# Kernel tuning notes

Hardware: AMD Instinct MI355X
Metric: run time of the kernel (lower is better)

The kernel has to match this reference:

```python
import jax, jax.numpy as jnp
import numpy as np
import math

DIMS = [2048, 1024, 512, 4096]
NH, DK, DV = 16, 64, 64
BS = 8192
D_MODEL = NH * DK  # 1024


def setup_inputs() -> dict:
    key = jax.random.key(0)
    ks = jax.random.split(key, 3 * len(DIMS) + 5)
    inp = {"input_data": jax.random.normal(ks[0], (BS, sum(DIMS)), jnp.float32)}
    ki = 1
    for i, d in enumerate(DIMS):
        inp[f"wq{i}"] = jax.random.normal(ks[ki], (NH * DK, d), jnp.float32) * 0.02; ki += 1
        inp[f"wk{i}"] = jax.random.normal(ks[ki], (NH * DK, d), jnp.float32) * 0.02; ki += 1
        inp[f"wv{i}"] = jax.random.normal(ks[ki], (NH * DV, d), jnp.float32) * 0.02; ki += 1
    inp["fc_w"] = jax.random.normal(ks[ki], (NH * DV, NH * DV), jnp.float32) * 0.02; ki += 1
    inp["fc_b"] = jax.random.normal(ks[ki], (NH * DV,), jnp.float32) * 0.02; ki += 1
    inp["ln_g"] = jnp.ones((NH * DV,), jnp.float32)
    inp["ln_b"] = jnp.zeros((NH * DV,), jnp.float32)
    return inp


def _forward(input_data, wqs, wks, wvs, fc_w, fc_b, ln_g, ln_b):
    bs = input_data.shape[0]
    M = len(DIMS)
    offs = np.cumsum([0] + DIMS)
    # per-modality projections; stack into [bs, M, NH*D]
    xs = [input_data[:, offs[i]:offs[i + 1]] for i in range(M)]
    q = jnp.stack([x @ w.T for x, w in zip(xs, wqs)], axis=1)  # [bs, M, NH*DK]
    k = jnp.stack([x @ w.T for x, w in zip(xs, wks)], axis=1)
    v = jnp.stack([x @ w.T for x, w in zip(xs, wvs)], axis=1)  # [bs, M, NH*DV]
    residual = v  # v.transpose(1,2).view == original stacked v
    qh = q.reshape(bs, M, NH, DK).transpose(0, 2, 1, 3)  # [bs, NH, M, DK]
    kh = k.reshape(bs, M, NH, DK).transpose(0, 2, 1, 3)
    vh = v.reshape(bs, M, NH, DV).transpose(0, 2, 1, 3)
    scores = jnp.einsum('bhqd,bhkd->bhqk', qh, kh) / math.sqrt(DK)
    attn = jax.nn.softmax(scores, axis=-1)  # [bs, NH, M, M]
    ctx = jnp.einsum('bhqk,bhkd->bhqd', attn, vh)  # [bs, NH, M, DV]
    ctx = ctx.transpose(0, 2, 1, 3).reshape(bs, M, NH * DV)
    out = ctx @ fc_w.T + fc_b  # dropout is identity (p=0 / eval)
    out = out + residual
    mu = jnp.mean(out, axis=-1, keepdims=True)
    var = jnp.var(out, axis=-1, keepdims=True)
    out = (out - mu) / jnp.sqrt(var + 1e-6) * ln_g + ln_b
    return out, attn


def reference(input_data, wq0, wk0, wv0, wq1, wk1, wv1, wq2, wk2, wv2,
              wq3, wk3, wv3, fc_w, fc_b, ln_g, ln_b):
    wqs = [wq0, wq1, wq2, wq3]
    wks = [wk0, wk1, wk2, wk3]
    wvs = [wv0, wv1, wv2, wv3]
    return _forward(input_data, wqs, wks, wvs, fc_w, fc_b, ln_g, ln_b)
```

## Files before the change

kernel.cpp:

```cpp
#include <hip/hip_runtime.h>


typedef unsigned short u16;
typedef short short8 __attribute__((ext_vector_type(8)));
typedef float f32x4 __attribute__((ext_vector_type(4)));

__device__ __forceinline__ u16 f2bf(float f) {
  unsigned u = __builtin_bit_cast(unsigned, f);
  u += 0x7FFFu + ((u >> 16) & 1u);
  return (u16)(u >> 16);
}
__device__ __forceinline__ float bf2f(u16 s) {
  return __builtin_bit_cast(float, ((unsigned)s) << 16);
}

__device__ __forceinline__ void gload16(const u16* g, u16* l) {
  __builtin_amdgcn_global_load_lds(
      (const __attribute__((address_space(1))) void*)g,
      (__attribute__((address_space(3))) void*)l, 16, 0, 0);
}

#define CFENCE asm volatile("" ::: "memory")

struct CArgs {
  const float* src[14];
  unsigned long dst[14];
  int blk0[14];
  int n4[14];
};

__global__ __launch_bounds__(256) void convall(CArgs a, u16* __restrict__ wsb) {
  int blk = blockIdx.x;
  int s = 0;
#pragma unroll
  for (int i = 1; i < 14; ++i) s = (blk >= a.blk0[i]) ? i : s;
  int li = (blk - a.blk0[s]) * 256 + threadIdx.x;
  if (li < a.n4[s]) {
    float4 v = ((const float4*)a.src[s])[li];
    ushort4 o;
    o.x = f2bf(v.x); o.y = f2bf(v.y); o.z = f2bf(v.z); o.w = f2bf(v.w);
    ((ushort4*)(wsb + a.dst[s]))[li] = o;
  }
}

template <int MODE>
__global__ __launch_bounds__(512, 2)
void gemm8(const u16* __restrict__ Abase, int lda,
           const u16* __restrict__ Wbase, u16* __restrict__ Cq,
           u16* __restrict__ Cpre, const float* __restrict__ bias,
           const u16* __restrict__ resid) {
  __shared__ __align__(16) u16 lds[65536];

  const int tid = threadIdx.x;
  const int w = tid >> 6, lane = tid & 63;
  const int lr = lane & 15, lk = lane >> 4;
  const int wm = w >> 2, wn = w & 3;

  int K, nt, bx, by, coff;
  const u16 *A, *B;
  if (MODE == 0) {
    int seg = blockIdx.x / 384;
    int r = blockIdx.x % 384;
    bx = r % 12; by = r / 12;
    K = 4096 >> seg; nt = 64 >> seg;
    int xo, wo, mod;
    switch (seg) {
      case 0:  xo = 3584; wo = 11010048; mod = 3; break;
      case 1:  xo = 0;    wo = 0;        mod = 0; break;
      case 2:  xo = 2048; wo = 6291456;  mod = 1; break;
      default: xo = 3072; wo = 9437184;  mod = 2; break;
    }
    coff = mod * 3072;
    A = Abase + xo;
    B = Wbase + wo;
  } else {
    bx = blockIdx.x & 3; by = blockIdx.x >> 2;
    K = 1024; nt = 16; coff = 0;
    A = Abase; B = Wbase;
  }
  const size_t brow = (size_t)by * 256;
  const int bcol = bx * 256;
  const u16* Ab = A + brow * (size_t)lda;
  const u16* Bb = B + (size_t)bcol * (size_t)K;

  f32x4 acc[8][4];
#pragma unroll
  for (int i = 0; i < 8; ++i)
#pragma unroll
    for (int j = 0; j < 4; ++j) acc[i][j] = (f32x4){0.f, 0.f, 0.f, 0.f};

  auto stageA = [&](int p, int half) {
    const int base = (p & 1) * 65536 + half * 16384;
    const int k0 = p * 64;
#pragma unroll
    for (int l = 0; l < 2; ++l) {
      int s = l * 8192 + tid * 16;
      int rw = s >> 7;
      int ck = ((s >> 4) & 7) ^ (rw & 7);
      int row = (rw & 63) + ((rw >> 6) << 7) + half * 64;
      gload16(Ab + (size_t)row * lda + k0 + ck * 8, &lds[(base + s) >> 1]);
    }
  };
  auto stageB = [&](int p, int half) {
    const int base = (p & 1) * 65536 + 32768 + half * 16384;
    const int k0 = p * 64;
#pragma unroll
    for (int l = 0; l < 2; ++l) {
      int s = l * 8192 + tid * 16;
      int rw = s >> 7;
      int ck = ((s >> 4) & 7) ^ (rw & 7);
      int col = (rw & 31) + ((rw >> 5) << 6) + half * 32;
      gload16(Bb + (size_t)col * (size_t)K + k0 + ck * 8, &lds[(base + s) >> 1]);
    }
  };

  auto ldA = [&](int t, int half, short8* dst) {
    const u16* lp = lds + (((t & 1) * 65536 + half * 16384) >> 1);
#pragma unroll
    for (int mi = 0; mi < 4; ++mi) {
      int rw = mi * 16 + lr + wm * 64;
#pragma unroll
      for (int ks = 0; ks < 2; ++ks) {
        int pc = (ks * 4 + lk) ^ (rw & 7);
        dst[mi * 2 + ks] = *(const short8*)(lp + rw * 64 + pc * 8);
      }
    }
  };
  auto ldB = [&](int t, int half, short8* dst) {
    const u16* lp = lds + (((t & 1) * 65536 + 32768 + half * 16384) >> 1);
#pragma unroll
    for (int ni = 0; ni < 2; ++ni) {
      int rw = ni * 16 + lr + wn * 32;
#pragma unroll
      for (int ks = 0; ks < 2; ++ks) {
        int pc = (ks * 4 + lk) ^ (rw & 7);
        dst[ni * 2 + ks] = *(const short8*)(lp + rw * 64 + pc * 8);
      }
    }
  };

  short8 af[8], bl[4], bh[4];
  auto MQ = [&](short8* a, short8* b, int mo, int no) {
#pragma unroll
    for (int mi = 0; mi < 4; ++mi)
#pragma unroll
      for (int ni = 0; ni < 2; ++ni) {
        acc[mo + mi][no + ni] = __builtin_amdgcn_mfma_f32_16x16x32_bf16(
            a[mi * 2 + 0], b[ni * 2 + 0], acc[mo + mi][no + ni], 0, 0, 0);
        acc[mo + mi][no + ni] = __builtin_amdgcn_mfma_f32_16x16x32_bf16(
            a[mi * 2 + 1], b[ni * 2 + 1], acc[mo + mi][no + ni], 0, 0, 0);
      }
  };

  stageA(0, 0); stageB(0, 0); stageB(0, 1); stageA(0, 1);
  asm volatile("s_waitcnt vmcnt(4)" ::: "memory");
  __builtin_amdgcn_s_barrier();
  CFENCE;

#pragma unroll 1
  for (int t = 0; t < nt; ++t) {
    const bool more = (t + 1 < nt);
    ldA(t, 0, af);
    ldB(t, 0, bl);
    if (more) stageA(t + 1, 0);
    CFENCE;
    __builtin_amdgcn_s_barrier();
    asm volatile("s_waitcnt lgkmcnt(0)" ::: "memory");
    __builtin_amdgcn_sched_barrier(0);
    __builtin_amdgcn_s_setprio(1);
    MQ(af, bl, 0, 0);
    __builtin_amdgcn_s_setprio(0);
    CFENCE;
    if (more) asm volatile("s_waitcnt vmcnt(4)" ::: "memory");
    else      asm volatile("s_waitcnt vmcnt(2)" ::: "memory");
    __builtin_amdgcn_s_barrier();
    CFENCE;
    ldB(t, 1, bh);
    if (more) stageB(t + 1, 0);
    CFENCE;
    __builtin_amdgcn_s_barrier();
    asm volatile("s_waitcnt lgkmcnt(0)" ::: "memory");
    __builtin_amdgcn_sched_barrier(0);
    __builtin_amdgcn_s_setprio(1);
    MQ(af, bh, 0, 2);
    __builtin_amdgcn_s_setprio(0);
    CFENCE;
    if (more) asm volatile("s_waitcnt vmcnt(4)" ::: "memory");
    else      asm volatile("s_waitcnt vmcnt(0)" ::: "memory");
    __builtin_amdgcn_s_barrier();
    CFENCE;
    ldA(t, 1, af);
    if (more) stageB(t + 1, 1);
    CFENCE;
    __builtin_amdgcn_s_barrier();
    asm volatile("s_waitcnt lgkmcnt(0)" ::: "memory");
    __builtin_amdgcn_sched_barrier(0);
    __builtin_amdgcn_s_setprio(1);
    MQ(af, bh, 4, 2);
    __builtin_amdgcn_s_setprio(0);
    CFENCE;
    __builtin_amdgcn_s_barrier();
    CFENCE;
    if (more) stageA(t + 1, 1);
    CFENCE;
    __builtin_amdgcn_s_barrier();
    __builtin_amdgcn_s_setprio(1);
    MQ(af, bl, 4, 0);
    __builtin_amdgcn_s_setprio(0);
    CFENCE;
    if (more) {
      asm volatile("s_waitcnt vmcnt(4)" ::: "memory");
      __builtin_amdgcn_s_barrier();
      CFENCE;
    }
  }

  if (MODE == 0) {
#pragma unroll
    for (int mi = 0; mi < 8; ++mi)
#pragma unroll
      for (int ni = 0; ni < 4; ++ni) {
        const int c = coff + bcol + wn * 64 + ni * 16 + lr;
#pragma unroll
        for (int j = 0; j < 4; ++j) {
          size_t r = brow + wm * 128 + mi * 16 + lk * 4 + j;
          Cq[r * 12288 + c] = f2bf(acc[mi][ni][j]);
        }
      }
  } else {
#pragma unroll
    for (int mi = 0; mi < 8; ++mi)
#pragma unroll
      for (int ni = 0; ni < 4; ++ni) {
        const int c = bcol + wn * 64 + ni * 16 + lr;
        const float bs = bias[c];
#pragma unroll
        for (int j = 0; j < 4; ++j) {
          size_t r = brow + wm * 128 + mi * 16 + lk * 4 + j;
          size_t ridx = (r >> 2) * 12288 + (r & 3) * 3072 + 2048 + c;
          Cpre[r * 1024 + c] = f2bf(acc[mi][ni][j] + bs + bf2f(resid[ridx]));
        }
      }
  }
}

__global__ __launch_bounds__(256) void attn_k(const u16* __restrict__ qkv,
                                              u16* __restrict__ ctxb,
                                              float* __restrict__ attn_out) {
  const int tid = threadIdx.x;
  const int l = tid & 63;
  const int wg = blockIdx.x * 4 + (tid >> 6);
  const int b = wg >> 2;
  const int h0 = (wg & 3) << 2;
  const size_t base = (size_t)b * 12288 + h0 * 64 + l * 4;

  float q[4][4], k[4][4], v[4][4];
#pragma unroll
  for (int m = 0; m < 4; ++m) {
    ushort4 uq = *(const ushort4*)(qkv + base + m * 3072);
    ushort4 uk = *(const ushort4*)(qkv + base + m * 3072 + 1024);
    ushort4 uv = *(const ushort4*)(qkv + base + m * 3072 + 2048);
    q[m][0] = bf2f(uq.x); q[m][1] = bf2f(uq.y); q[m][2] = bf2f(uq.z); q[m][3] = bf2f(uq.w);
    k[m][0] = bf2f(uk.x); k[m][1] = bf2f(uk.y); k[m][2] = bf2f(uk.z); k[m][3] = bf2f(uk.w);
    v[m][0] = bf2f(uv.x); v[m][1] = bf2f(uv.y); v[m][2] = bf2f(uv.z); v[m][3] = bf2f(uv.w);
  }

  float s[16];
#pragma unroll
  for (int i = 0; i < 4; ++i)
#pragma unroll
    for (int j = 0; j < 4; ++j) {
      float acc = q[i][0] * k[j][0];
      acc += q[i][1] * k[j][1];
      acc += q[i][2] * k[j][2];
      acc += q[i][3] * k[j][3];
      s[i * 4 + j] = acc;
    }
#pragma unroll
  for (int off = 1; off < 16; off <<= 1) {
#pragma unroll
    for (int t = 0; t < 16; ++t) s[t] += __shfl_xor(s[t], off);
  }

  float a[16];
#pragma unroll
  for (int i = 0; i < 4; ++i) {
    float s0 = s[i * 4 + 0] * 0.125f, s1 = s[i * 4 + 1] * 0.125f;
    float s2 = s[i * 4 + 2] * 0.125f, s3 = s[i * 4 + 3] * 0.125f;
    float m = fmaxf(fmaxf(s0, s1), fmaxf(s2, s3));
    float e0 = __expf(s0 - m), e1 = __expf(s1 - m);
    float e2 = __expf(s2 - m), e3 = __expf(s3 - m);
    float inv = 1.0f / (e0 + e1 + e2 + e3);
    a[i * 4 + 0] = e0 * inv; a[i * 4 + 1] = e1 * inv;
    a[i * 4 + 2] = e2 * inv; a[i * 4 + 3] = e3 * inv;
  }

#pragma unroll
  for (int i = 0; i < 4; ++i) {
    float c0 = a[i*4+0]*v[0][0] + a[i*4+1]*v[1][0] + a[i*4+2]*v[2][0] + a[i*4+3]*v[3][0];
    float c1 = a[i*4+0]*v[0][1] + a[i*4+1]*v[1][1] + a[i*4+2]*v[2][1] + a[i*4+3]*v[3][1];
    float c2 = a[i*4+0]*v[0][2] + a[i*4+1]*v[1][2] + a[i*4+2]*v[2][2] + a[i*4+3]*v[3][2];
    float c3 = a[i*4+0]*v[0][3] + a[i*4+1]*v[1][3] + a[i*4+2]*v[2][3] + a[i*4+3]*v[3][3];
    ushort4 o;
    o.x = f2bf(c0); o.y = f2bf(c1); o.z = f2bf(c2); o.w = f2bf(c3);
    *(ushort4*)(ctxb + (size_t)b * 4096 + i * 1024 + h0 * 64 + l * 4) = o;
  }

  int sel = l & 15;
  float val = a[0];
#pragma unroll
  for (int t = 1; t < 16; ++t) val = (sel == t) ? a[t] : val;
  attn_out[(size_t)b * 256 + h0 * 16 + l] = val;
}

__global__ __launch_bounds__(256) void ln_k(const u16* __restrict__ pre,
                                            const float* __restrict__ g,
                                            const float* __restrict__ b,
                                            float* __restrict__ out) {
  int row = blockIdx.x;
  int tid = threadIdx.x;
  ushort4 u = *(const ushort4*)(pre + (size_t)row * 1024 + tid * 4);
  float x0 = bf2f(u.x), x1 = bf2f(u.y), x2 = bf2f(u.z), x3 = bf2f(u.w);
  float s = x0 + x1 + x2 + x3;
  float s2 = x0 * x0 + x1 * x1 + x2 * x2 + x3 * x3;
#pragma unroll
  for (int off = 32; off; off >>= 1) {
    s += __shfl_xor(s, off);
    s2 += __shfl_xor(s2, off);
  }
  __shared__ float r1[4], r2[4];
  int w = tid >> 6, lane = tid & 63;
  if (lane == 0) { r1[w] = s; r2[w] = s2; }
  __syncthreads();
  s = r1[0] + r1[1] + r1[2] + r1[3];
  s2 = r2[0] + r2[1] + r2[2] + r2[3];
  float mu = s * (1.0f / 1024.0f);
  float inv = rsqrtf(s2 * (1.0f / 1024.0f) - mu * mu + 1e-6f);
  float4 gv = *(const float4*)(g + tid * 4);
  float4 bv = *(const float4*)(b + tid * 4);
  float4 o;
  o.x = (x0 - mu) * inv * gv.x + bv.x;
  o.y = (x1 - mu) * inv * gv.y + bv.y;
  o.z = (x2 - mu) * inv * gv.z + bv.z;
  o.w = (x3 - mu) * inv * gv.w + bv.w;
  *(float4*)(out + (size_t)row * 1024 + tid * 4) = o;
}

extern "C" void kernel_launch(void* const* d_in, const int* in_sizes, int n_in,
                              void* d_out, int out_size, void* d_ws,
                              size_t ws_size, hipStream_t stream) {
  const float* fcb = (const float*)d_in[14];
  const float* lng = (const float*)d_in[15];
  const float* lnb = (const float*)d_in[16];

  u16* wsb = (u16*)d_ws;
  u16* xb = wsb;
  u16* wb = xb + 62914560;
  u16* qkv = wb + 24641536;
  u16* ctxb = qkv + 100663296;
  u16* pre = wsb;
  float* outp = (float*)d_out;
  float* attn_out = outp + 33554432;

  static const unsigned long woff[13] = {
      0,        2097152,  4194304,
      6291456,  7340032,  8388608,
      9437184,  9961472,  10485760,
      11010048, 15204352, 19398656,
      23592960};
  static const int wn4[13] = {524288, 524288, 524288, 262144, 262144, 262144,
                              131072, 131072, 131072, 1048576, 1048576, 1048576,
                              262144};

  CArgs ca;
  ca.src[0] = (const float*)d_in[0];
  ca.dst[0] = 0;
  ca.n4[0] = 62914560 / 4;
  ca.blk0[0] = 0;
  int nb = ca.n4[0] / 256;
  for (int i = 0; i < 13; ++i) {
    ca.src[i + 1] = (const float*)d_in[1 + i];
    ca.dst[i + 1] = 62914560ul + woff[i];
    ca.n4[i + 1] = wn4[i];
    ca.blk0[i + 1] = nb;
    nb += (wn4[i] + 255) / 256;
  }
  convall<<<dim3(nb), 256, 0, stream>>>(ca, wsb);

  gemm8<0><<<dim3(1536), 512, 0, stream>>>(xb, 7680, wb, qkv, nullptr, nullptr,
                                           nullptr);

  attn_k<<<dim3(8192), 256, 0, stream>>>(qkv, ctxb, attn_out);

  gemm8<1><<<dim3(512), 512, 0, stream>>>(ctxb, 1024, wb + 23592960, nullptr,
                                          pre, fcb, qkv);

  ln_k<<<dim3(32768), 256, 0, stream>>>(pre, lng, lnb, outp);
}
```

Baseline: 617.0 us.

## Switch GEMM to 32x32x16 MFMA and use nontemporal loads/stores throughout

The GEMM inner product moves from 16x16x32 to 32x32x16 bf16 MFMA instructions. LDS fragment loads and the epilogue indexing are reworked to match the 32x32 output layout, with fewer and larger accumulator tiles. Separately, streaming global loads and stores in the conversion, attention, LayerNorm and GEMM epilogue kernels become nontemporal to cut cache pollution. The larger MFMA reduces instruction count and LDS reads per flop. The epilogue still issues scalar 16-bit stores with a strided row pattern, and the nontemporal hints could hurt if data such as qkv would otherwise be reused from cache.

```diff
diff --git a/kernel.cpp b/kernel.cpp
--- a/kernel.cpp
+++ b/kernel.cpp
@@ -3,7 +3,9 @@
 
 typedef unsigned short u16;
 typedef short short8 __attribute__((ext_vector_type(8)));
+typedef unsigned short u16x4 __attribute__((ext_vector_type(4)));
 typedef float f32x4 __attribute__((ext_vector_type(4)));
+typedef float f32x16 __attribute__((ext_vector_type(16)));
 
 __device__ __forceinline__ u16 f2bf(float f) {
   unsigned u = __builtin_bit_cast(unsigned, f);
@@ -36,10 +38,10 @@
   for (int i = 1; i < 14; ++i) s = (blk >= a.blk0[i]) ? i : s;
   int li = (blk - a.blk0[s]) * 256 + threadIdx.x;
   if (li < a.n4[s]) {
-    float4 v = ((const float4*)a.src[s])[li];
-    ushort4 o;
+    f32x4 v = __builtin_nontemporal_load((const f32x4*)a.src[s] + li);
+    u16x4 o;
     o.x = f2bf(v.x); o.y = f2bf(v.y); o.z = f2bf(v.z); o.w = f2bf(v.w);
-    ((ushort4*)(wsb + a.dst[s]))[li] = o;
+    __builtin_nontemporal_store(o, (u16x4*)(wsb + a.dst[s]) + li);
   }
 }
 
@@ -53,7 +55,7 @@
 
   const int tid = threadIdx.x;
   const int w = tid >> 6, lane = tid & 63;
-  const int lr = lane & 15, lk = lane >> 4;
+  const int l31 = lane & 31, lk5 = lane >> 5;
   const int wm = w >> 2, wn = w & 3;
 
   int K, nt, bx, by, coff;
@@ -83,11 +85,11 @@
   const u16* Ab = A + brow * (size_t)lda;
   const u16* Bb = B + (size_t)bcol * (size_t)K;
 
-  f32x4 acc[8][4];
-#pragma unroll
-  for (int i = 0; i < 8; ++i)
-#pragma unroll
-    for (int j = 0; j < 4; ++j) acc[i][j] = (f32x4){0.f, 0.f, 0.f, 0.f};
+  f32x16 acc[4][2];
+#pragma unroll
+  for (int i = 0; i < 4; ++i)
+#pragma unroll
+    for (int j = 0; j < 2; ++j) acc[i][j] = (f32x16)(0.f);
 
   auto stageA = [&](int p, int half) {
     const int base = (p & 1) * 65536 + half * 16384;
@@ -117,39 +119,33 @@
   auto ldA = [&](int t, int half, short8* dst) {
     const u16* lp = lds + (((t & 1) * 65536 + half * 16384) >> 1);
 #pragma unroll
-    for (int mi = 0; mi < 4; ++mi) {
-      int rw = mi * 16 + lr + wm * 64;
-#pragma unroll
-      for (int ks = 0; ks < 2; ++ks) {
-        int pc = (ks * 4 + lk) ^ (rw & 7);
-        dst[mi * 2 + ks] = *(const short8*)(lp + rw * 64 + pc * 8);
+    for (int mi2 = 0; mi2 < 2; ++mi2) {
+      int rw = wm * 64 + mi2 * 32 + l31;
+#pragma unroll
+      for (int ks = 0; ks < 4; ++ks) {
+        int pc = (ks * 2 + lk5) ^ (rw & 7);
+        dst[mi2 * 4 + ks] = *(const short8*)(lp + rw * 64 + pc * 8);
       }
     }
   };
   auto ldB = [&](int t, int half, short8* dst) {
     const u16* lp = lds + (((t & 1) * 65536 + 32768 + half * 16384) >> 1);
-#pragma unroll
-    for (int ni = 0; ni < 2; ++ni) {
-      int rw = ni * 16 + lr + wn * 32;
-#pragma unroll
-      for (int ks = 0; ks < 2; ++ks) {
-        int pc = (ks * 4 + lk) ^ (rw & 7);
-        dst[ni * 2 + ks] = *(const short8*)(lp + rw * 64 + pc * 8);
-      }
+    int rw = wn * 32 + l31;
+#pragma unroll
+    for (int ks = 0; ks < 4; ++ks) {
+      int pc = (ks * 2 + lk5) ^ (rw & 7);
+      dst[ks] = *(const short8*)(lp + rw * 64 + pc * 8);
     }
   };
 
   short8 af[8], bl[4], bh[4];
   auto MQ = [&](short8* a, short8* b, int mo, int no) {
 #pragma unroll
-    for (int mi = 0; mi < 4; ++mi)
-#pragma unroll
-      for (int ni = 0; ni < 2; ++ni) {
-        acc[mo + mi][no + ni] = __builtin_amdgcn_mfma_f32_16x16x32_bf16(
-            a[mi * 2 + 0], b[ni * 2 + 0], acc[mo + mi][no + ni], 0, 0, 0);
-        acc[mo + mi][no + ni] = __builtin_amdgcn_mfma_f32_16x16x32_bf16(
-            a[mi * 2 + 1], b[ni * 2 + 1], acc[mo + mi][no + ni], 0, 0, 0);
-      }
+    for (int mi2 = 0; mi2 < 2; ++mi2)
+#pragma unroll
+      for (int ks = 0; ks < 4; ++ks)
+        acc[mo + mi2][no] = __builtin_amdgcn_mfma_f32_32x32x16_bf16(
+            a[mi2 * 4 + ks], b[ks], acc[mo + mi2][no], 0, 0, 0);
   };
 
   stageA(0, 0); stageB(0, 0); stageB(0, 1); stageA(0, 1);
@@ -182,7 +178,7 @@
     asm volatile("s_waitcnt lgkmcnt(0)" ::: "memory");
     __builtin_amdgcn_sched_barrier(0);
     __builtin_amdgcn_s_setprio(1);
-    MQ(af, bh, 0, 2);
+    MQ(af, bh, 0, 1);
     __builtin_amdgcn_s_setprio(0);
     CFENCE;
     if (more) asm volatile("s_waitcnt vmcnt(4)" ::: "memory");
@@ -196,7 +192,7 @@
     asm volatile("s_waitcnt lgkmcnt(0)" ::: "memory");
     __builtin_amdgcn_sched_barrier(0);
     __builtin_amdgcn_s_setprio(1);
-    MQ(af, bh, 4, 2);
+    MQ(af, bh, 2, 1);
     __builtin_amdgcn_s_setprio(0);
     CFENCE;
     __builtin_amdgcn_s_barrier();
@@ -205,7 +201,7 @@
     CFENCE;
     __builtin_amdgcn_s_barrier();
     __builtin_amdgcn_s_setprio(1);
-    MQ(af, bl, 4, 0);
+    MQ(af, bl, 2, 0);
     __builtin_amdgcn_s_setprio(0);
     CFENCE;
     if (more) {
@@ -217,28 +213,33 @@
 
   if (MODE == 0) {
 #pragma unroll
-    for (int mi = 0; mi < 8; ++mi)
-#pragma unroll
-      for (int ni = 0; ni < 4; ++ni) {
-        const int c = coff + bcol + wn * 64 + ni * 16 + lr;
-#pragma unroll
-        for (int j = 0; j < 4; ++j) {
-          size_t r = brow + wm * 128 + mi * 16 + lk * 4 + j;
-          Cq[r * 12288 + c] = f2bf(acc[mi][ni][j]);
+    for (int mi = 0; mi < 4; ++mi)
+#pragma unroll
+      for (int ni = 0; ni < 2; ++ni) {
+        const int c = coff + bcol + wn * 64 + ni * 32 + l31;
+        const size_t rb = brow + wm * 128 + mi * 32 + lk5 * 4;
+#pragma unroll
+        for (int reg = 0; reg < 16; ++reg) {
+          size_t r = rb + (reg & 3) + 8 * (reg >> 2);
+          __builtin_nontemporal_store(f2bf(acc[mi][ni][reg]),
+                                      &Cq[r * 12288 + c]);
         }
       }
   } else {
 #pragma unroll
-    for (int mi = 0; mi < 8; ++mi)
-#pragma unroll
-      for (int ni = 0; ni < 4; ++ni) {
-        const int c = bcol + wn * 64 + ni * 16 + lr;
+    for (int mi = 0; mi < 4; ++mi)
+#pragma unroll
+      for (int ni = 0; ni < 2; ++ni) {
+        const int c = bcol + wn * 64 + ni * 32 + l31;
         const float bs = bias[c];
-#pragma unroll
-        for (int j = 0; j < 4; ++j) {
-          size_t r = brow + wm * 128 + mi * 16 + lk * 4 + j;
+        const size_t rb = brow + wm * 128 + mi * 32 + lk5 * 4;
+#pragma unroll
+        for (int reg = 0; reg < 16; ++reg) {
+          size_t r = rb + (reg & 3) + 8 * (reg >> 2);
           size_t ridx = (r >> 2) * 12288 + (r & 3) * 3072 + 2048 + c;
-          Cpre[r * 1024 + c] = f2bf(acc[mi][ni][j] + bs + bf2f(resid[ridx]));
+          u16 rv = __builtin_nontemporal_load(&resid[ridx]);
+          __builtin_nontemporal_store(f2bf(acc[mi][ni][reg] + bs + bf2f(rv)),
+                                      &Cpre[r * 1024 + c]);
         }
       }
   }
@@ -257,9 +258,9 @@
   float q[4][4], k[4][4], v[4][4];
 #pragma unroll
   for (int m = 0; m < 4; ++m) {
-    ushort4 uq = *(const ushort4*)(qkv + base + m * 3072);
-    ushort4 uk = *(const ushort4*)(qkv + base + m * 3072 + 1024);
-    ushort4 uv = *(const ushort4*)(qkv + base + m * 3072 + 2048);
+    u16x4 uq = __builtin_nontemporal_load((const u16x4*)(qkv + base + m * 3072));
+    u16x4 uk = __builtin_nontemporal_load((const u16x4*)(qkv + base + m * 3072 + 1024));
+    u16x4 uv = __builtin_nontemporal_load((const u16x4*)(qkv + base + m * 3072 + 2048));
     q[m][0] = bf2f(uq.x); q[m][1] = bf2f(uq.y); q[m][2] = bf2f(uq.z); q[m][3] = bf2f(uq.w);
     k[m][0] = bf2f(uk.x); k[m][1] = bf2f(uk.y); k[m][2] = bf2f(uk.z); k[m][3] = bf2f(uk.w);
     v[m][0] = bf2f(uv.x); v[m][1] = bf2f(uv.y); v[m][2] = bf2f(uv.z); v[m][3] = bf2f(uv.w);
@@ -301,16 +302,16 @@
     float c1 = a[i*4+0]*v[0][1] + a[i*4+1]*v[1][1] + a[i*4+2]*v[2][1] + a[i*4+3]*v[3][1];
     float c2 = a[i*4+0]*v[0][2] + a[i*4+1]*v[1][2] + a[i*4+2]*v[2][2] + a[i*4+3]*v[3][2];
     float c3 = a[i*4+0]*v[0][3] + a[i*4+1]*v[1][3] + a[i*4+2]*v[2][3] + a[i*4+3]*v[3][3];
-    ushort4 o;
+    u16x4 o;
     o.x = f2bf(c0); o.y = f2bf(c1); o.z = f2bf(c2); o.w = f2bf(c3);
-    *(ushort4*)(ctxb + (size_t)b * 4096 + i * 1024 + h0 * 64 + l * 4) = o;
+    *(u16x4*)(ctxb + (size_t)b * 4096 + i * 1024 + h0 * 64 + l * 4) = o;
   }
 
   int sel = l & 15;
   float val = a[0];
 #pragma unroll
   for (int t = 1; t < 16; ++t) val = (sel == t) ? a[t] : val;
-  attn_out[(size_t)b * 256 + h0 * 16 + l] = val;
+  __builtin_nontemporal_store(val, &attn_out[(size_t)b * 256 + h0 * 16 + l]);
 }
 
 __global__ __launch_bounds__(256) void ln_k(const u16* __restrict__ pre,
@@ -319,7 +320,8 @@
                                             float* __restrict__ out) {
   int row = blockIdx.x;
   int tid = threadIdx.x;
-  ushort4 u = *(const ushort4*)(pre + (size_t)row * 1024 + tid * 4);
+  u16x4 u = __builtin_nontemporal_load(
+      (const u16x4*)(pre + (size_t)row * 1024 + tid * 4));
   float x0 = bf2f(u.x), x1 = bf2f(u.y), x2 = bf2f(u.z), x3 = bf2f(u.w);
   float s = x0 + x1 + x2 + x3;
   float s2 = x0 * x0 + x1 * x1 + x2 * x2 + x3 * x3;
@@ -338,12 +340,12 @@
   float inv = rsqrtf(s2 * (1.0f / 1024.0f) - mu * mu + 1e-6f);
   float4 gv = *(const float4*)(g + tid * 4);
   float4 bv = *(const float4*)(b + tid * 4);
-  float4 o;
+  f32x4 o;
   o.x = (x0 - mu) * inv * gv.x + bv.x;
   o.y = (x1 - mu) * inv * gv.y + bv.y;
   o.z = (x2 - mu) * inv * gv.z + bv.z;
   o.w = (x3 - mu) * inv * gv.w + bv.w;
-  *(float4*)(out + (size_t)row * 1024 + tid * 4) = o;
+  __builtin_nontemporal_store(o, (f32x4*)(out + (size_t)row * 1024 + tid * 4));
 }
 
 extern "C" void kernel_launch(void* const* d_in, const int* in_sizes, int n_in,
```

After: 712.1 us. 15.4% more time.
